# Performance work log

Measured on AMD Instinct MI355X. Metric: run time of the kernel, lower is better.

The kernel has to match this reference:

```python
import jax, jax.numpy as jnp
import numpy as np

REG_WEIGHT = 1e-4
N_LAYERS = 3


def setup_inputs() -> dict:
    key = jax.random.key(0)
    ks = jax.random.split(key, 7)
    n_users, n_items, d = 100000, 50000, 64
    E, B = 1600000, 4096
    return {
        "user_table": jax.random.normal(ks[0], (n_users, d), dtype=jnp.float32) * 0.01,
        "item_table": jax.random.normal(ks[1], (n_items, d), dtype=jnp.float32) * 0.01,
        "edge_u": jax.random.randint(ks[2], (E,), 0, n_users, dtype=jnp.int32),
        "edge_i": jax.random.randint(ks[3], (E,), 0, n_items, dtype=jnp.int32),
        "users": jax.random.randint(ks[4], (B,), 0, n_users, dtype=jnp.int32),
        "pos_items": jax.random.randint(ks[5], (B,), 0, n_items, dtype=jnp.int32),
        "neg_items": jax.random.randint(ks[6], (B,), 0, n_items, dtype=jnp.int32),
    }


def _lightgcn_embeddings(user_table, item_table, edge_u, edge_i):
    n_users, n_items = user_table.shape[0], item_table.shape[0]
    N = n_users + n_items
    E = edge_u.shape[0]
    ones = jnp.ones((E,), dtype=user_table.dtype)
    # symmetric normalization D^{-1/2} A D^{-1/2} on the bipartite graph
    deg_u = jax.ops.segment_sum(ones, edge_u, num_segments=n_users)
    deg_i = jax.ops.segment_sum(ones, edge_i, num_segments=n_items)
    w = jax.lax.rsqrt(jnp.maximum(deg_u[edge_u] * deg_i[edge_i], 1.0))
    # symmetric edge list over the stacked [users; items] node set
    rows = jnp.concatenate([edge_u, edge_i + n_users])
    cols = jnp.concatenate([edge_i + n_users, edge_u])
    vals = jnp.concatenate([w, w])[:, None]

    x = jnp.concatenate([user_table, item_table], axis=0)  # [N, d]
    acc = x
    for _ in range(N_LAYERS):
        x = jax.ops.segment_sum(x[cols] * vals, rows, num_segments=N)
        acc = acc + x
    final = acc / jnp.asarray(N_LAYERS + 1, dtype=x.dtype)
    return final[:n_users], final[n_users:]


def reference(user_table, item_table, edge_u, edge_i, users, pos_items, neg_items):
    user_emb_all, item_emb_all = _lightgcn_embeddings(user_table, item_table, edge_u, edge_i)
    u_emb = user_emb_all[users]
    pos_i_emb = item_emb_all[pos_items]
    neg_i_emb = item_emb_all[neg_items]
    pos_scores = jnp.sum(u_emb * pos_i_emb, axis=-1)
    neg_scores = jnp.sum(u_emb * neg_i_emb, axis=-1)
    # L2 regularization on the layer-0 (table) embeddings
    u0 = user_table[users]
    p0 = item_table[pos_items]
    n0 = item_table[neg_items]
    reg_loss = REG_WEIGHT * (jnp.sum(u0 * u0) + jnp.sum(p0 * p0) + jnp.sum(n0 * n0))
    reg_loss = reg_loss / users.shape[0]
    return pos_scores, neg_scores, reg_loss
```

## Files before the change

kernel.cpp:

```cpp
#include <hip/hip_runtime.h>
#include <hip/hip_fp16.h>

#define THREADS 256
#define BIN_C 4096
#define NBMAX 400
#define CAP 4608
#define SH_U 8
#define SH_I 7
#define CPAD 16
#define T_TILES 8
#define TSH_U 13
#define TSH_I 14

__global__ void bin_kernel(const int* __restrict__ eu, const int* __restrict__ ei,
                           int* __restrict__ bcnt_u, int* __restrict__ bcnt_i,
                           int* __restrict__ binu, int* __restrict__ bini,
                           int E, int nbu, int nbi) {
    __shared__ int hist_u[NBMAX], hist_i[NBMAX];
    __shared__ int base_u[NBMAX], base_i[NBMAX];
    int tid = threadIdx.x;
    int e0 = blockIdx.x * BIN_C;
    if (e0 >= E) return;
    int cnt = min(BIN_C, E - e0);

    for (int b = tid; b < NBMAX; b += THREADS) { hist_u[b] = 0; hist_i[b] = 0; }
    __syncthreads();

    int u[16], v[16];
    #pragma unroll
    for (int j = 0; j < 16; ++j) {
        int k = tid + j * THREADS;
        if (k < cnt) { u[j] = eu[e0 + k]; v[j] = ei[e0 + k]; }
        else         { u[j] = -1; v[j] = -1; }
    }
    #pragma unroll
    for (int j = 0; j < 16; ++j) {
        if (u[j] >= 0) {
            atomicAdd(&hist_u[u[j] >> SH_U], 1);
            atomicAdd(&hist_i[v[j] >> SH_I], 1);
        }
    }
    __syncthreads();
    for (int b = tid; b < NBMAX; b += THREADS) {
        int cu = hist_u[b], ci = hist_i[b];
        base_u[b] = (cu > 0 && b < nbu) ? atomicAdd(&bcnt_u[(size_t)b * CPAD], cu) : 0;
        base_i[b] = (ci > 0 && b < nbi) ? atomicAdd(&bcnt_i[(size_t)b * CPAD], ci) : 0;
        hist_u[b] = 0; hist_i[b] = 0;
    }
    __syncthreads();
    #pragma unroll
    for (int j = 0; j < 16; ++j) {
        if (u[j] >= 0) {
            int bu = u[j] >> SH_U;
            int pu = base_u[bu] + atomicAdd(&hist_u[bu], 1);
            if (pu < CAP) binu[(size_t)bu * CAP + pu] = ((u[j] & 255) << 16) | v[j];
            int bi = v[j] >> SH_I;
            int pi = base_i[bi] + atomicAdd(&hist_i[bi], 1);
            if (pi < CAP) bini[(size_t)bi * CAP + pi] = ((v[j] & 127) << 17) | u[j];
        }
    }
}

__global__ void place(const int* __restrict__ bcnt_u, const int* __restrict__ bcnt_i,
                      const int* __restrict__ binu, const int* __restrict__ bini,
                      int* __restrict__ offu, int* __restrict__ offi,
                      int* __restrict__ du, int* __restrict__ di,
                      float* __restrict__ rsdu, float* __restrict__ rsdi,
                      int* __restrict__ entu, int* __restrict__ enti,
                      int* __restrict__ curs,
                      int nbu, int nU, int nI) {
    __shared__ int stash[CAP];
    __shared__ int bin_cnt[THREADS * T_TILES];
    __shared__ int node_base[THREADS];
    __shared__ int wsum[4];
    __shared__ int bob_sh;
    int b = blockIdx.x;
    bool isU = (b < nbu);
    const int* bin; int base_node, nn, count;
    int *off, *deg, *ent; float* rsd;
    int losh, tsh, lomask;
    if (isU) {
        bin = binu + (size_t)b * CAP;
        base_node = b << SH_U; nn = min(256, nU - base_node);
        count = min(bcnt_u[(size_t)b * CPAD], CAP);
        off = offu; deg = du; rsd = rsdu; ent = entu;
        losh = 16; tsh = TSH_U; lomask = 0xFFFF;
    } else {
        int b2 = b - nbu;
        bin = bini + (size_t)b2 * CAP;
        base_node = b2 << SH_I; nn = min(128, nI - base_node);
        count = min(bcnt_i[(size_t)b2 * CPAD], CAP);
        off = offi; deg = di; rsd = rsdi; ent = enti;
        losh = 17; tsh = TSH_I; lomask = 0x1FFFF;
    }
    int tid = threadIdx.x;
    #pragma unroll
    for (int t = 0; t < T_TILES; ++t) bin_cnt[tid + t * THREADS] = 0;
    __syncthreads();
    for (int k = tid; k < count; k += THREADS) {
        int p = bin[k];
        stash[k] = p;
        int key = ((p >> losh) << 3) | ((p & lomask) >> tsh);
        atomicAdd(&bin_cnt[key], 1);
    }
    __syncthreads();
    int c = 0;
    {
        int base = tid * T_TILES;
        #pragma unroll
        for (int t = 0; t < T_TILES; ++t) {
            int v = bin_cnt[base + t];
            bin_cnt[base + t] = c;
            c += v;
        }
    }
    int seg = (c + 15) & ~15;
    int lane = tid & 63, wid = tid >> 6;
    int inc = seg;
    #pragma unroll
    for (int ofs = 1; ofs < 64; ofs <<= 1) {
        int t = __shfl_up(inc, ofs);
        if (lane >= ofs) inc += t;
    }
    if (lane == 63) wsum[wid] = inc;
    __syncthreads();
    int wofs = 0;
    #pragma unroll
    for (int w = 0; w < 4; ++w) wofs += (w < wid) ? wsum[w] : 0;
    int incl = inc + wofs;
    int excl = incl - seg;
    if (tid == THREADS - 1) bob_sh = atomicAdd(&curs[isU ? 0 : 1], incl);
    __syncthreads();
    int bob = bob_sh;
    node_base[tid] = excl;
    if (tid < nn) {
        off[base_node + tid] = bob + excl;
        deg[base_node + tid] = c;
        rsd[base_node + tid] = rsqrtf(fmaxf((float)c, 1.0f));
    }
    __syncthreads();
    #pragma unroll
    for (int t = 0; t < T_TILES; ++t) {
        int k = tid + t * THREADS;
        bin_cnt[k] += node_base[k >> 3];
    }
    __syncthreads();
    for (int k = tid; k < count; k += THREADS) {
        int p = stash[k];
        int key = ((p >> losh) << 3) | ((p & lomask) >> tsh);
        int sl = atomicAdd(&bin_cnt[key], 1);
        ent[bob + sl] = p & lomask;
    }
}

__global__ void conv16all(const float* __restrict__ ut, const float* __restrict__ it,
                          __half* __restrict__ dst, int nU16, int ntot16) {
    int stride = gridDim.x * blockDim.x;
    for (int i = blockIdx.x * blockDim.x + threadIdx.x; i < ntot16; i += stride) {
        const float* src = (i < nU16) ? (ut + (size_t)i * 4) : (it + (size_t)(i - nU16) * 4);
        float4 v = *reinterpret_cast<const float4*>(src);
        __half2 h0 = __float22half2_rn(make_float2(v.x, v.y));
        __half2 h1 = __float22half2_rn(make_float2(v.z, v.w));
        uint2 st;
        st.x = *reinterpret_cast<unsigned*>(&h0);
        st.y = *reinterpret_cast<unsigned*>(&h1);
        *reinterpret_cast<uint2*>(dst + (size_t)i * 4) = st;
    }
}

__global__ void prop16(const __half* __restrict__ x,
                       const int* __restrict__ offu, const int* __restrict__ offi,
                       const int* __restrict__ du, const int* __restrict__ di,
                       const float* __restrict__ rsdu, const float* __restrict__ rsdi,
                       const int* __restrict__ entu, const int* __restrict__ enti,
                       __half* __restrict__ y, int nU, int N) {
    int node = blockIdx.x * (THREADS >> 3) + (threadIdx.x >> 3);
    int lane = threadIdx.x & 7;
    if (node >= N) return;
    const int* ent; const __half* src; const float* rsdn;
    int beg, dg; float rs;
    if (node < nU) {
        beg = offu[node]; dg = du[node]; rs = rsdu[node];
        ent = entu; src = x + ((size_t)nU << 6); rsdn = rsdi;
    } else {
        int i = node - nU;
        beg = offi[i]; dg = di[i]; rs = rsdi[i];
        ent = enti; src = x; rsdn = rsdu;
    }
    float a0=0,a1=0,a2=0,a3=0,a4=0,a5=0,a6=0,a7=0;
    for (int k0 = 0; k0 < dg; k0 += 8) {
        int me = (k0 + lane < dg) ? ent[beg + k0 + lane] : 0;
        #pragma unroll
        for (int j = 0; j < 8; ++j) {
            if (k0 + j < dg) {
                int nbr = __shfl(me, j, 8);
                float w = rsdn[nbr];
                uint4 r = *reinterpret_cast<const uint4*>(src + ((size_t)nbr << 6) + (lane << 3));
                __half2 h0 = *reinterpret_cast<__half2*>(&r.x);
                __half2 h1 = *reinterpret_cast<__half2*>(&r.y);
                __half2 h2 = *reinterpret_cast<__half2*>(&r.z);
                __half2 h3 = *reinterpret_cast<__half2*>(&r.w);
                float2 f0 = __half22float2(h0), f1 = __half22float2(h1);
                float2 f2 = __half22float2(h2), f3 = __half22float2(h3);
                a0 += w * f0.x; a1 += w * f0.y; a2 += w * f1.x; a3 += w * f1.y;
                a4 += w * f2.x; a5 += w * f2.y; a6 += w * f3.x; a7 += w * f3.y;
            }
        }
    }
    __half2 o0 = __float22half2_rn(make_float2(a0 * rs, a1 * rs));
    __half2 o1 = __float22half2_rn(make_float2(a2 * rs, a3 * rs));
    __half2 o2 = __float22half2_rn(make_float2(a4 * rs, a5 * rs));
    __half2 o3 = __float22half2_rn(make_float2(a6 * rs, a7 * rs));
    uint4 st;
    st.x = *reinterpret_cast<unsigned*>(&o0);
    st.y = *reinterpret_cast<unsigned*>(&o1);
    st.z = *reinterpret_cast<unsigned*>(&o2);
    st.w = *reinterpret_cast<unsigned*>(&o3);
    *reinterpret_cast<uint4*>(y + ((size_t)node << 6) + (lane << 3)) = st;
}

__global__ void prop_sel_acc(const __half* __restrict__ x,
                             const int* __restrict__ users, const int* __restrict__ pos,
                             const int* __restrict__ neg,
                             const int* __restrict__ offu, const int* __restrict__ offi,
                             const int* __restrict__ du, const int* __restrict__ di,
                             const float* __restrict__ rsdu, const float* __restrict__ rsdi,
                             const int* __restrict__ entu, const int* __restrict__ enti,
                             float* __restrict__ sel, int B, int nU) {
    int r = blockIdx.x * (THREADS >> 3) + (threadIdx.x >> 3);
    int lane = threadIdx.x & 7;
    if (r >= 3 * B) return;
    int which = r / B, b = r - which * B;
    const int* ent; const __half* src; const float* rsdn;
    int beg, dg; float rs; size_t selfrow;
    if (which == 0) {
        int u = users[b];
        beg = offu[u]; dg = du[u]; rs = rsdu[u];
        ent = entu; src = x + ((size_t)nU << 6); rsdn = rsdi;
        selfrow = (size_t)u << 6;
    } else {
        int i = (which == 1) ? pos[b] : neg[b];
        beg = offi[i]; dg = di[i]; rs = rsdi[i];
        ent = enti; src = x; rsdn = rsdu;
        selfrow = (size_t)(nU + i) << 6;
    }
    float a0=0,a1=0,a2=0,a3=0,a4=0,a5=0,a6=0,a7=0;
    for (int k0 = 0; k0 < dg; k0 += 8) {
        int me = (k0 + lane < dg) ? ent[beg + k0 + lane] : 0;
        #pragma unroll
        for (int j = 0; j < 8; ++j) {
            if (k0 + j < dg) {
                int nbr = __shfl(me, j, 8);
                float w = rsdn[nbr];
                uint4 rv = *reinterpret_cast<const uint4*>(src + ((size_t)nbr << 6) + (lane << 3));
                __half2 h0 = *reinterpret_cast<__half2*>(&rv.x);
                __half2 h1 = *reinterpret_cast<__half2*>(&rv.y);
                __half2 h2 = *reinterpret_cast<__half2*>(&rv.z);
                __half2 h3 = *reinterpret_cast<__half2*>(&rv.w);
                float2 f0 = __half22float2(h0), f1 = __half22float2(h1);
                float2 f2 = __half22float2(h2), f3 = __half22float2(h3);
                a0 += w * f0.x; a1 += w * f0.y; a2 += w * f1.x; a3 += w * f1.y;
                a4 += w * f2.x; a5 += w * f2.y; a6 += w * f3.x; a7 += w * f3.y;
            }
        }
    }
    uint4 rv = *reinterpret_cast<const uint4*>(x + selfrow + (lane << 3));
    __half2 h0 = *reinterpret_cast<__half2*>(&rv.x);
    __half2 h1 = *reinterpret_cast<__half2*>(&rv.y);
    __half2 h2 = *reinterpret_cast<__half2*>(&rv.z);
    __half2 h3 = *reinterpret_cast<__half2*>(&rv.w);
    float2 s0 = __half22float2(h0), s1 = __half22float2(h1);
    float2 s2 = __half22float2(h2), s3 = __half22float2(h3);
    float* s = sel + ((size_t)r << 6) + (lane << 3);
    float4 d0 = *reinterpret_cast<float4*>(s);
    float4 d1 = *reinterpret_cast<float4*>(s + 4);
    d0.x += s0.x + rs * a0; d0.y += s0.y + rs * a1;
    d0.z += s1.x + rs * a2; d0.w += s1.y + rs * a3;
    d1.x += s2.x + rs * a4; d1.y += s2.y + rs * a5;
    d1.z += s3.x + rs * a6; d1.w += s3.y + rs * a7;
    *reinterpret_cast<float4*>(s) = d0;
    *reinterpret_cast<float4*>(s + 4) = d1;
}

__global__ void selreg(const float* __restrict__ ut, const float* __restrict__ it,
                       const int* __restrict__ users, const int* __restrict__ pos,
                       const int* __restrict__ neg,
                       float* __restrict__ sel, float* __restrict__ out_reg,
                       int B, float scale) {
    int r = blockIdx.x * (THREADS >> 4) + (threadIdx.x >> 4);
    int t = threadIdx.x & 15;
    float ssq = 0.f;
    if (r < 3 * B) {
        int which = r / B, b = r - which * B;
        const float* base; int idx;
        if (which == 0)      { base = ut; idx = users[b]; }
        else if (which == 1) { base = it; idx = pos[b]; }
        else                 { base = it; idx = neg[b]; }
        float4 v = *reinterpret_cast<const float4*>(base + ((size_t)idx << 6) + t * 4);
        *reinterpret_cast<float4*>(sel + ((size_t)r << 6) + t * 4) = v;
        ssq = v.x * v.x + v.y * v.y + v.z * v.z + v.w * v.w;
    }
    #pragma unroll
    for (int ofs = 32; ofs; ofs >>= 1) ssq += __shfl_down(ssq, ofs);
    if ((threadIdx.x & 63) == 0) atomicAdd(out_reg, ssq * scale);
}

__global__ void sel_acc16(const __half* __restrict__ x,
                          const int* __restrict__ users, const int* __restrict__ pos,
                          const int* __restrict__ neg, float* __restrict__ sel, int B, int nU) {
    int r = blockIdx.x * (THREADS >> 3) + (threadIdx.x >> 3);
    int lane = threadIdx.x & 7;
    if (r >= 3 * B) return;
    int which = r / B, b = r - which * B;
    size_t row;
    if (which == 0)      row = (size_t)users[b];
    else if (which == 1) row = (size_t)nU + pos[b];
    else                 row = (size_t)nU + neg[b];
    uint4 rv = *reinterpret_cast<const uint4*>(x + (row << 6) + (lane << 3));
    __half2 h0 = *reinterpret_cast<__half2*>(&rv.x);
    __half2 h1 = *reinterpret_cast<__half2*>(&rv.y);
    __half2 h2 = *reinterpret_cast<__half2*>(&rv.z);
    __half2 h3 = *reinterpret_cast<__half2*>(&rv.w);
    float2 f0 = __half22float2(h0), f1 = __half22float2(h1);
    float2 f2 = __half22float2(h2), f3 = __half22float2(h3);
    float* s = sel + ((size_t)r << 6) + (lane << 3);
    float4 d0 = *reinterpret_cast<float4*>(s);
    float4 d1 = *reinterpret_cast<float4*>(s + 4);
    d0.x += f0.x; d0.y += f0.y; d0.z += f1.x; d0.w += f1.y;
    d1.x += f2.x; d1.y += f2.y; d1.z += f3.x; d1.w += f3.y;
    *reinterpret_cast<float4*>(s) = d0;
    *reinterpret_cast<float4*>(s + 4) = d1;
}

__global__ void score(const float* __restrict__ sel, float* __restrict__ out, int B) {
    int b = blockIdx.x * (THREADS >> 6) + (threadIdx.x >> 6);
    int lane = threadIdx.x & 63;
    if (b >= B) return;
    float u = sel[((size_t)b << 6) + lane];
    float p = sel[((size_t)(B + b) << 6) + lane];
    float n = sel[((size_t)(2 * B + b) << 6) + lane];
    float ps = u * p, ns = u * n;
    for (int ofs = 32; ofs; ofs >>= 1) {
        ps += __shfl_down(ps, ofs);
        ns += __shfl_down(ns, ofs);
    }
    if (lane == 0) {
        out[b]     = ps * (1.0f / 16.0f);
        out[B + b] = ns * (1.0f / 16.0f);
    }
}

extern "C" void kernel_launch(void* const* d_in, const int* in_sizes, int n_in,
                              void* d_out, int out_size, void* d_ws, size_t ws_size,
                              hipStream_t stream) {
    const float* ut   = (const float*)d_in[0];
    const float* it   = (const float*)d_in[1];
    const int* eu     = (const int*)d_in[2];
    const int* ei     = (const int*)d_in[3];
    const int* users  = (const int*)d_in[4];
    const int* pos    = (const int*)d_in[5];
    const int* neg    = (const int*)d_in[6];
    int nU = in_sizes[0] / 64;
    int nI = in_sizes[1] / 64;
    int E  = in_sizes[2];
    int B  = in_sizes[4];
    int N  = nU + nI;
    float* out = (float*)d_out;

    int nbu = (nU + 255) >> SH_U;
    int nbi = (nI + 127) >> SH_I;

    char* ws = (char*)d_ws;
    size_t cursor = 0;
    auto alloc = [&](size_t bytes) -> void* {
        cursor = (cursor + 255) & ~(size_t)255;
        void* p = ws + cursor;
        cursor += bytes;
        return p;
    };
    int*   bcnt_u = (int*)alloc((size_t)nbu * CPAD * 4);
    int*   bcnt_i = (int*)alloc((size_t)nbi * CPAD * 4);
    int*   curs   = (int*)alloc(2 * 4);
    size_t zero_span = cursor;
    int*   binu = (int*)alloc((size_t)nbu * CAP * 4);
    int*   bini = (int*)alloc((size_t)nbi * CAP * 4);
    int*   offu = (int*)alloc((size_t)nU * 4);
    int*   offi = (int*)alloc((size_t)nI * 4);
    int*   du   = (int*)alloc((size_t)nU * 4);
    int*   di   = (int*)alloc((size_t)nI * 4);
    float* rsdu = (float*)alloc((size_t)nU * 4);
    float* rsdi = (float*)alloc((size_t)nI * 4);
    int*   entu = (int*)alloc(((size_t)E + (size_t)nbu * 256 * 16) * 4);
    int*   enti = (int*)alloc(((size_t)E + (size_t)nbi * 128 * 16) * 4);
    __half* xA  = (__half*)alloc((size_t)N * 64 * 2);
    __half* xB  = (__half*)alloc((size_t)N * 64 * 2);
    float* sel  = (float*)alloc((size_t)3 * B * 64 * 4);

    hipMemsetAsync(d_ws, 0, zero_span, stream);
    hipMemsetAsync(out + 2 * B, 0, sizeof(float), stream);

    conv16all<<<2048, THREADS, 0, stream>>>(ut, it, xA, nU * 16, N * 16);

    int nchunks = (E + BIN_C - 1) / BIN_C;
    bin_kernel<<<nchunks, THREADS, 0, stream>>>(eu, ei, bcnt_u, bcnt_i, binu, bini, E, nbu, nbi);
    place<<<nbu + nbi, THREADS, 0, stream>>>(bcnt_u, bcnt_i, binu, bini,
                                             offu, offi, du, di, rsdu, rsdi, entu, enti,
                                             curs, nbu, nU, nI);

    selreg<<<(3 * B + 15) / 16, THREADS, 0, stream>>>(ut, it, users, pos, neg, sel,
                                                      out + 2 * B, B, 1e-4f / (float)B);

    int gridSel16 = (3 * B * 8 + THREADS - 1) / THREADS;
    int gridProp = (N * 8 + THREADS - 1) / THREADS;
    prop16<<<gridProp, THREADS, 0, stream>>>(xA, offu, offi, du, di, rsdu, rsdi, entu, enti, xB, nU, N);
    sel_acc16<<<gridSel16, THREADS, 0, stream>>>(xB, users, pos, neg, sel, B, nU);
    prop16<<<gridProp, THREADS, 0, stream>>>(xB, offu, offi, du, di, rsdu, rsdi, entu, enti, xA, nU, N);
    prop_sel_acc<<<gridSel16, THREADS, 0, stream>>>(xA, users, pos, neg, offu, offi, du, di,
                                                    rsdu, rsdi, entu, enti, sel, B, nU);

    score<<<(B + 3) / 4, THREADS, 0, stream>>>(sel, out, B);
}
```

Measured before the change: 284.7 us.

## Fuse propagation layers and scoring into one cooperative kernel with grid syncs

Replaces the chain of prop16, sel_acc16, prop_sel_acc and score launches with a single persistent cooperative kernel that runs each phase in grid-stride loops and separates phases with grid.sync(). The second-layer select-accumulate now runs in the same phase as the second propagation. A separate bucket_off kernel computes per-bucket output offsets up front, and place uses a shared-memory scan instead of a per-block atomic cursor. This aims to remove kernel-launch gaps and tail effects between the short dependent stages, at the cost of grid-wide barrier overhead and a grid sized from occupancy queries, which may lower per-phase parallelism.

```diff
diff --git a/kernel.cpp b/kernel.cpp
--- a/kernel.cpp
+++ b/kernel.cpp
@@ -1,5 +1,8 @@
 #include <hip/hip_runtime.h>
 #include <hip/hip_fp16.h>
+#include <hip/hip_cooperative_groups.h>
+
+namespace cg = cooperative_groups;
 
 #define THREADS 256
 #define BIN_C 4096
@@ -11,147 +14,6 @@
 #define T_TILES 8
 #define TSH_U 13
 #define TSH_I 14
-
-__global__ void bin_kernel(const int* __restrict__ eu, const int* __restrict__ ei,
-                           int* __restrict__ bcnt_u, int* __restrict__ bcnt_i,
-                           int* __restrict__ binu, int* __restrict__ bini,
-                           int E, int nbu, int nbi) {
-    __shared__ int hist_u[NBMAX], hist_i[NBMAX];
-    __shared__ int base_u[NBMAX], base_i[NBMAX];
-    int tid = threadIdx.x;
-    int e0 = blockIdx.x * BIN_C;
-    if (e0 >= E) return;
-    int cnt = min(BIN_C, E - e0);
-
-    for (int b = tid; b < NBMAX; b += THREADS) { hist_u[b] = 0; hist_i[b] = 0; }
-    __syncthreads();
-
-    int u[16], v[16];
-    #pragma unroll
-    for (int j = 0; j < 16; ++j) {
-        int k = tid + j * THREADS;
-        if (k < cnt) { u[j] = eu[e0 + k]; v[j] = ei[e0 + k]; }
-        else         { u[j] = -1; v[j] = -1; }
-    }
-    #pragma unroll
-    for (int j = 0; j < 16; ++j) {
-        if (u[j] >= 0) {
-            atomicAdd(&hist_u[u[j] >> SH_U], 1);
-            atomicAdd(&hist_i[v[j] >> SH_I], 1);
-        }
-    }
-    __syncthreads();
-    for (int b = tid; b < NBMAX; b += THREADS) {
-        int cu = hist_u[b], ci = hist_i[b];
-        base_u[b] = (cu > 0 && b < nbu) ? atomicAdd(&bcnt_u[(size_t)b * CPAD], cu) : 0;
-        base_i[b] = (ci > 0 && b < nbi) ? atomicAdd(&bcnt_i[(size_t)b * CPAD], ci) : 0;
-        hist_u[b] = 0; hist_i[b] = 0;
-    }
-    __syncthreads();
-    #pragma unroll
-    for (int j = 0; j < 16; ++j) {
-        if (u[j] >= 0) {
-            int bu = u[j] >> SH_U;
-            int pu = base_u[bu] + atomicAdd(&hist_u[bu], 1);
-            if (pu < CAP) binu[(size_t)bu * CAP + pu] = ((u[j] & 255) << 16) | v[j];
-            int bi = v[j] >> SH_I;
-            int pi = base_i[bi] + atomicAdd(&hist_i[bi], 1);
-            if (pi < CAP) bini[(size_t)bi * CAP + pi] = ((v[j] & 127) << 17) | u[j];
-        }
-    }
-}
-
-__global__ void place(const int* __restrict__ bcnt_u, const int* __restrict__ bcnt_i,
-                      const int* __restrict__ binu, const int* __restrict__ bini,
-                      int* __restrict__ offu, int* __restrict__ offi,
-                      int* __restrict__ du, int* __restrict__ di,
-                      float* __restrict__ rsdu, float* __restrict__ rsdi,
-                      int* __restrict__ entu, int* __restrict__ enti,
-                      int* __restrict__ curs,
-                      int nbu, int nU, int nI) {
-    __shared__ int stash[CAP];
-    __shared__ int bin_cnt[THREADS * T_TILES];
-    __shared__ int node_base[THREADS];
-    __shared__ int wsum[4];
-    __shared__ int bob_sh;
-    int b = blockIdx.x;
-    bool isU = (b < nbu);
-    const int* bin; int base_node, nn, count;
-    int *off, *deg, *ent; float* rsd;
-    int losh, tsh, lomask;
-    if (isU) {
-        bin = binu + (size_t)b * CAP;
-        base_node = b << SH_U; nn = min(256, nU - base_node);
-        count = min(bcnt_u[(size_t)b * CPAD], CAP);
-        off = offu; deg = du; rsd = rsdu; ent = entu;
-        losh = 16; tsh = TSH_U; lomask = 0xFFFF;
-    } else {
-        int b2 = b - nbu;
-        bin = bini + (size_t)b2 * CAP;
-        base_node = b2 << SH_I; nn = min(128, nI - base_node);
-        count = min(bcnt_i[(size_t)b2 * CPAD], CAP);
-        off = offi; deg = di; rsd = rsdi; ent = enti;
-        losh = 17; tsh = TSH_I; lomask = 0x1FFFF;
-    }
-    int tid = threadIdx.x;
-    #pragma unroll
-    for (int t = 0; t < T_TILES; ++t) bin_cnt[tid + t * THREADS] = 0;
-    __syncthreads();
-    for (int k = tid; k < count; k += THREADS) {
-        int p = bin[k];
-        stash[k] = p;
-        int key = ((p >> losh) << 3) | ((p & lomask) >> tsh);
-        atomicAdd(&bin_cnt[key], 1);
-    }
-    __syncthreads();
-    int c = 0;
-    {
-        int base = tid * T_TILES;
-        #pragma unroll
-        for (int t = 0; t < T_TILES; ++t) {
-            int v = bin_cnt[base + t];
-            bin_cnt[base + t] = c;
-            c += v;
-        }
-    }
-    int seg = (c + 15) & ~15;
-    int lane = tid & 63, wid = tid >> 6;
-    int inc = seg;
-    #pragma unroll
-    for (int ofs = 1; ofs < 64; ofs <<= 1) {
-        int t = __shfl_up(inc, ofs);
-        if (lane >= ofs) inc += t;
-    }
-    if (lane == 63) wsum[wid] = inc;
-    __syncthreads();
-    int wofs = 0;
-    #pragma unroll
-    for (int w = 0; w < 4; ++w) wofs += (w < wid) ? wsum[w] : 0;
-    int incl = inc + wofs;
-    int excl = incl - seg;
-    if (tid == THREADS - 1) bob_sh = atomicAdd(&curs[isU ? 0 : 1], incl);
-    __syncthreads();
-    int bob = bob_sh;
-    node_base[tid] = excl;
-    if (tid < nn) {
-        off[base_node + tid] = bob + excl;
-        deg[base_node + tid] = c;
-        rsd[base_node + tid] = rsqrtf(fmaxf((float)c, 1.0f));
-    }
-    __syncthreads();
-    #pragma unroll
-    for (int t = 0; t < T_TILES; ++t) {
-        int k = tid + t * THREADS;
-        bin_cnt[k] += node_base[k >> 3];
-    }
-    __syncthreads();
-    for (int k = tid; k < count; k += THREADS) {
-        int p = stash[k];
-        int key = ((p >> losh) << 3) | ((p & lomask) >> tsh);
-        int sl = atomicAdd(&bin_cnt[key], 1);
-        ent[bob + sl] = p & lomask;
-    }
-}
 
 __global__ void conv16all(const float* __restrict__ ut, const float* __restrict__ it,
                           __half* __restrict__ dst, int nU16, int ntot16) {
@@ -168,15 +30,186 @@
     }
 }
 
-__global__ void prop16(const __half* __restrict__ x,
-                       const int* __restrict__ offu, const int* __restrict__ offi,
-                       const int* __restrict__ du, const int* __restrict__ di,
-                       const float* __restrict__ rsdu, const float* __restrict__ rsdi,
-                       const int* __restrict__ entu, const int* __restrict__ enti,
-                       __half* __restrict__ y, int nU, int N) {
-    int node = blockIdx.x * (THREADS >> 3) + (threadIdx.x >> 3);
-    int lane = threadIdx.x & 7;
-    if (node >= N) return;
+__global__ void bin_kernel(const int* __restrict__ eu, const int* __restrict__ ei,
+                           int* __restrict__ bcnt_u, int* __restrict__ bcnt_i,
+                           int* __restrict__ binu, int* __restrict__ bini,
+                           int E, int nbu, int nbi) {
+    __shared__ int hist_u[NBMAX], hist_i[NBMAX];
+    __shared__ int base_u[NBMAX], base_i[NBMAX];
+    int tid = threadIdx.x;
+    int e0 = blockIdx.x * BIN_C;
+    if (e0 >= E) return;
+    int cnt = min(BIN_C, E - e0);
+    for (int b = tid; b < NBMAX; b += THREADS) { hist_u[b] = 0; hist_i[b] = 0; }
+    __syncthreads();
+    int u[16], v[16];
+    #pragma unroll
+    for (int j = 0; j < 16; ++j) {
+        int k = tid + j * THREADS;
+        if (k < cnt) { u[j] = eu[e0 + k]; v[j] = ei[e0 + k]; }
+        else         { u[j] = -1; v[j] = -1; }
+    }
+    #pragma unroll
+    for (int j = 0; j < 16; ++j) {
+        if (u[j] >= 0) {
+            atomicAdd(&hist_u[u[j] >> SH_U], 1);
+            atomicAdd(&hist_i[v[j] >> SH_I], 1);
+        }
+    }
+    __syncthreads();
+    for (int b = tid; b < NBMAX; b += THREADS) {
+        int cu = hist_u[b], ci = hist_i[b];
+        base_u[b] = (cu > 0 && b < nbu) ? atomicAdd(&bcnt_u[(size_t)b * CPAD], cu) : 0;
+        base_i[b] = (ci > 0 && b < nbi) ? atomicAdd(&bcnt_i[(size_t)b * CPAD], ci) : 0;
+        hist_u[b] = 0; hist_i[b] = 0;
+    }
+    __syncthreads();
+    #pragma unroll
+    for (int j = 0; j < 16; ++j) {
+        if (u[j] >= 0) {
+            int bu = u[j] >> SH_U;
+            int pu = base_u[bu] + atomicAdd(&hist_u[bu], 1);
+            if (pu < CAP) binu[(size_t)bu * CAP + pu] = ((u[j] & 255) << 16) | v[j];
+            int bi = v[j] >> SH_I;
+            int pi = base_i[bi] + atomicAdd(&hist_i[bi], 1);
+            if (pi < CAP) bini[(size_t)bi * CAP + pi] = ((v[j] & 127) << 17) | u[j];
+        }
+    }
+}
+
+__global__ void bucket_off(const int* __restrict__ bcnt, int* __restrict__ bo,
+                           int* __restrict__ cursor, int nb, int pad) {
+    int idx = blockIdx.x * blockDim.x + threadIdx.x;
+    int lane = threadIdx.x & 63;
+    int d = 0;
+    if (idx < nb) d = min(bcnt[(size_t)idx * CPAD], CAP) + pad;
+    int s = d;
+    #pragma unroll
+    for (int ofs = 1; ofs < 64; ofs <<= 1) {
+        int t = __shfl_up(s, ofs);
+        if (lane >= ofs) s += t;
+    }
+    int total = __shfl(s, 63);
+    int base = 0;
+    if (lane == 63) base = atomicAdd(cursor, total);
+    base = __shfl(base, 63);
+    if (idx < nb) bo[idx] = base + s - d;
+}
+
+__global__ void place(const int* __restrict__ bcnt_u, const int* __restrict__ bcnt_i,
+                      const int* __restrict__ bo_u, const int* __restrict__ bo_i,
+                      const int* __restrict__ binu, const int* __restrict__ bini,
+                      int* __restrict__ offu, int* __restrict__ offi,
+                      int* __restrict__ du, int* __restrict__ di,
+                      float* __restrict__ rsdu, float* __restrict__ rsdi,
+                      int* __restrict__ entu, int* __restrict__ enti,
+                      int nbu, int nU, int nI) {
+    __shared__ int stash[CAP];
+    __shared__ int bin_cnt[THREADS * T_TILES];
+    __shared__ int scan[THREADS];
+    __shared__ int node_base[THREADS];
+    int b = blockIdx.x;
+    bool isU = (b < nbu);
+    const int* bin; int base_node, nn, count, bob;
+    int *off, *deg, *ent; float* rsd;
+    int losh, tsh;
+    if (isU) {
+        bin = binu + (size_t)b * CAP;
+        base_node = b << SH_U; nn = min(256, nU - base_node);
+        count = min(bcnt_u[(size_t)b * CPAD], CAP); bob = bo_u[b];
+        off = offu; deg = du; rsd = rsdu; ent = entu;
+        losh = 16; tsh = TSH_U;
+    } else {
+        int b2 = b - nbu;
+        bin = bini + (size_t)b2 * CAP;
+        base_node = b2 << SH_I; nn = min(128, nI - base_node);
+        count = min(bcnt_i[(size_t)b2 * CPAD], CAP); bob = bo_i[b2];
+        off = offi; deg = di; rsd = rsdi; ent = enti;
+        losh = 17; tsh = TSH_I;
+    }
+    int lomask = (1 << losh) - 1;
+    int tid = threadIdx.x;
+    #pragma unroll
+    for (int t = 0; t < T_TILES; ++t) bin_cnt[tid + t * THREADS] = 0;
+    __syncthreads();
+    for (int k = tid; k < count; k += THREADS) {
+        int p = bin[k];
+        stash[k] = p;
+        int key = ((p >> losh) << 3) | ((p & lomask) >> tsh);
+        atomicAdd(&bin_cnt[key], 1);
+    }
+    __syncthreads();
+    int c = 0;
+    {
+        int base = tid * T_TILES;
+        #pragma unroll
+        for (int t = 0; t < T_TILES; ++t) {
+            int v = bin_cnt[base + t];
+            bin_cnt[base + t] = c;
+            c += v;
+        }
+    }
+    int seg = (c + 15) & ~15;
+    scan[tid] = seg;
+    __syncthreads();
+    #pragma unroll
+    for (int ofs = 1; ofs < THREADS; ofs <<= 1) {
+        int t = (tid >= ofs) ? scan[tid - ofs] : 0;
+        __syncthreads();
+        scan[tid] += t;
+        __syncthreads();
+    }
+    int excl = scan[tid] - seg;
+    node_base[tid] = excl;
+    if (tid < nn) {
+        off[base_node + tid] = bob + excl;
+        deg[base_node + tid] = c;
+        rsd[base_node + tid] = rsqrtf(fmaxf((float)c, 1.0f));
+    }
+    __syncthreads();
+    #pragma unroll
+    for (int t = 0; t < T_TILES; ++t) {
+        int k = tid + t * THREADS;
+        bin_cnt[k] += node_base[k >> 3];
+    }
+    __syncthreads();
+    for (int k = tid; k < count; k += THREADS) {
+        int p = stash[k];
+        int key = ((p >> losh) << 3) | ((p & lomask) >> tsh);
+        int sl = atomicAdd(&bin_cnt[key], 1);
+        ent[bob + sl] = p & lomask;
+    }
+}
+
+__global__ void selreg(const float* __restrict__ ut, const float* __restrict__ it,
+                       const int* __restrict__ users, const int* __restrict__ pos,
+                       const int* __restrict__ neg,
+                       float* __restrict__ sel, float* __restrict__ out_reg,
+                       int B, float scale) {
+    int r = blockIdx.x * (THREADS >> 4) + (threadIdx.x >> 4);
+    int t = threadIdx.x & 15;
+    float ssq = 0.f;
+    if (r < 3 * B) {
+        int which = r / B, b = r - which * B;
+        const float* base; int idx;
+        if (which == 0)      { base = ut; idx = users[b]; }
+        else if (which == 1) { base = it; idx = pos[b]; }
+        else                 { base = it; idx = neg[b]; }
+        float4 v = *reinterpret_cast<const float4*>(base + ((size_t)idx << 6) + t * 4);
+        *reinterpret_cast<float4*>(sel + ((size_t)r << 6) + t * 4) = v;
+        ssq = v.x * v.x + v.y * v.y + v.z * v.z + v.w * v.w;
+    }
+    #pragma unroll
+    for (int ofs = 32; ofs; ofs >>= 1) ssq += __shfl_down(ssq, ofs);
+    if ((threadIdx.x & 63) == 0) atomicAdd(out_reg, ssq * scale);
+}
+
+__device__ __forceinline__ void prop_node(const __half* __restrict__ x,
+                                          const int* __restrict__ offu, const int* __restrict__ offi,
+                                          const int* __restrict__ du, const int* __restrict__ di,
+                                          const float* __restrict__ rsdu, const float* __restrict__ rsdi,
+                                          const int* __restrict__ entu, const int* __restrict__ enti,
+                                          __half* __restrict__ y, int nU, int node, int lane) {
     const int* ent; const __half* src; const float* rsdn;
     int beg, dg; float rs;
     if (node < nU) {
@@ -219,98 +252,10 @@
     *reinterpret_cast<uint4*>(y + ((size_t)node << 6) + (lane << 3)) = st;
 }
 
-__global__ void prop_sel_acc(const __half* __restrict__ x,
-                             const int* __restrict__ users, const int* __restrict__ pos,
-                             const int* __restrict__ neg,
-                             const int* __restrict__ offu, const int* __restrict__ offi,
-                             const int* __restrict__ du, const int* __restrict__ di,
-                             const float* __restrict__ rsdu, const float* __restrict__ rsdi,
-                             const int* __restrict__ entu, const int* __restrict__ enti,
-                             float* __restrict__ sel, int B, int nU) {
-    int r = blockIdx.x * (THREADS >> 3) + (threadIdx.x >> 3);
-    int lane = threadIdx.x & 7;
-    if (r >= 3 * B) return;
-    int which = r / B, b = r - which * B;
-    const int* ent; const __half* src; const float* rsdn;
-    int beg, dg; float rs; size_t selfrow;
-    if (which == 0) {
-        int u = users[b];
-        beg = offu[u]; dg = du[u]; rs = rsdu[u];
-        ent = entu; src = x + ((size_t)nU << 6); rsdn = rsdi;
-        selfrow = (size_t)u << 6;
-    } else {
-        int i = (which == 1) ? pos[b] : neg[b];
-        beg = offi[i]; dg = di[i]; rs = rsdi[i];
-        ent = enti; src = x; rsdn = rsdu;
-        selfrow = (size_t)(nU + i) << 6;
-    }
-    float a0=0,a1=0,a2=0,a3=0,a4=0,a5=0,a6=0,a7=0;
-    for (int k0 = 0; k0 < dg; k0 += 8) {
-        int me = (k0 + lane < dg) ? ent[beg + k0 + lane] : 0;
-        #pragma unroll
-        for (int j = 0; j < 8; ++j) {
-            if (k0 + j < dg) {
-                int nbr = __shfl(me, j, 8);
-                float w = rsdn[nbr];
-                uint4 rv = *reinterpret_cast<const uint4*>(src + ((size_t)nbr << 6) + (lane << 3));
-                __half2 h0 = *reinterpret_cast<__half2*>(&rv.x);
-                __half2 h1 = *reinterpret_cast<__half2*>(&rv.y);
-                __half2 h2 = *reinterpret_cast<__half2*>(&rv.z);
-                __half2 h3 = *reinterpret_cast<__half2*>(&rv.w);
-                float2 f0 = __half22float2(h0), f1 = __half22float2(h1);
-                float2 f2 = __half22float2(h2), f3 = __half22float2(h3);
-                a0 += w * f0.x; a1 += w * f0.y; a2 += w * f1.x; a3 += w * f1.y;
-                a4 += w * f2.x; a5 += w * f2.y; a6 += w * f3.x; a7 += w * f3.y;
-            }
-        }
-    }
-    uint4 rv = *reinterpret_cast<const uint4*>(x + selfrow + (lane << 3));
-    __half2 h0 = *reinterpret_cast<__half2*>(&rv.x);
-    __half2 h1 = *reinterpret_cast<__half2*>(&rv.y);
-    __half2 h2 = *reinterpret_cast<__half2*>(&rv.z);
-    __half2 h3 = *reinterpret_cast<__half2*>(&rv.w);
-    float2 s0 = __half22float2(h0), s1 = __half22float2(h1);
-    float2 s2 = __half22float2(h2), s3 = __half22float2(h3);
-    float* s = sel + ((size_t)r << 6) + (lane << 3);
-    float4 d0 = *reinterpret_cast<float4*>(s);
-    float4 d1 = *reinterpret_cast<float4*>(s + 4);
-    d0.x += s0.x + rs * a0; d0.y += s0.y + rs * a1;
-    d0.z += s1.x + rs * a2; d0.w += s1.y + rs * a3;
-    d1.x += s2.x + rs * a4; d1.y += s2.y + rs * a5;
-    d1.z += s3.x + rs * a6; d1.w += s3.y + rs * a7;
-    *reinterpret_cast<float4*>(s) = d0;
-    *reinterpret_cast<float4*>(s + 4) = d1;
-}
-
-__global__ void selreg(const float* __restrict__ ut, const float* __restrict__ it,
-                       const int* __restrict__ users, const int* __restrict__ pos,
-                       const int* __restrict__ neg,
-                       float* __restrict__ sel, float* __restrict__ out_reg,
-                       int B, float scale) {
-    int r = blockIdx.x * (THREADS >> 4) + (threadIdx.x >> 4);
-    int t = threadIdx.x & 15;
-    float ssq = 0.f;
-    if (r < 3 * B) {
-        int which = r / B, b = r - which * B;
-        const float* base; int idx;
-        if (which == 0)      { base = ut; idx = users[b]; }
-        else if (which == 1) { base = it; idx = pos[b]; }
-        else                 { base = it; idx = neg[b]; }
-        float4 v = *reinterpret_cast<const float4*>(base + ((size_t)idx << 6) + t * 4);
-        *reinterpret_cast<float4*>(sel + ((size_t)r << 6) + t * 4) = v;
-        ssq = v.x * v.x + v.y * v.y + v.z * v.z + v.w * v.w;
-    }
-    #pragma unroll
-    for (int ofs = 32; ofs; ofs >>= 1) ssq += __shfl_down(ssq, ofs);
-    if ((threadIdx.x & 63) == 0) atomicAdd(out_reg, ssq * scale);
-}
-
-__global__ void sel_acc16(const __half* __restrict__ x,
-                          const int* __restrict__ users, const int* __restrict__ pos,
-                          const int* __restrict__ neg, float* __restrict__ sel, int B, int nU) {
-    int r = blockIdx.x * (THREADS >> 3) + (threadIdx.x >> 3);
-    int lane = threadIdx.x & 7;
-    if (r >= 3 * B) return;
+__device__ __forceinline__ void selacc_row(const __half* __restrict__ x,
+                                           const int* __restrict__ users, const int* __restrict__ pos,
+                                           const int* __restrict__ neg,
+                                           float* __restrict__ sel, int B, int nU, int r, int lane) {
     int which = r / B, b = r - which * B;
     size_t row;
     if (which == 0)      row = (size_t)users[b];
@@ -332,21 +277,110 @@
     *reinterpret_cast<float4*>(s + 4) = d1;
 }
 
-__global__ void score(const float* __restrict__ sel, float* __restrict__ out, int B) {
-    int b = blockIdx.x * (THREADS >> 6) + (threadIdx.x >> 6);
-    int lane = threadIdx.x & 63;
-    if (b >= B) return;
-    float u = sel[((size_t)b << 6) + lane];
-    float p = sel[((size_t)(B + b) << 6) + lane];
-    float n = sel[((size_t)(2 * B + b) << 6) + lane];
-    float ps = u * p, ns = u * n;
-    for (int ofs = 32; ofs; ofs >>= 1) {
-        ps += __shfl_down(ps, ofs);
-        ns += __shfl_down(ns, ofs);
-    }
-    if (lane == 0) {
-        out[b]     = ps * (1.0f / 16.0f);
-        out[B + b] = ns * (1.0f / 16.0f);
+__device__ __forceinline__ void propselacc_row(const __half* __restrict__ x,
+                                               const int* __restrict__ users, const int* __restrict__ pos,
+                                               const int* __restrict__ neg,
+                                               const int* __restrict__ offu, const int* __restrict__ offi,
+                                               const int* __restrict__ du, const int* __restrict__ di,
+                                               const float* __restrict__ rsdu, const float* __restrict__ rsdi,
+                                               const int* __restrict__ entu, const int* __restrict__ enti,
+                                               float* __restrict__ sel, int B, int nU, int r, int lane) {
+    int which = r / B, b = r - which * B;
+    const int* ent; const __half* src; const float* rsdn;
+    int beg, dg; float rs; size_t selfrow;
+    if (which == 0) {
+        int u = users[b];
+        beg = offu[u]; dg = du[u]; rs = rsdu[u];
+        ent = entu; src = x + ((size_t)nU << 6); rsdn = rsdi;
+        selfrow = (size_t)u << 6;
+    } else {
+        int i = (which == 1) ? pos[b] : neg[b];
+        beg = offi[i]; dg = di[i]; rs = rsdi[i];
+        ent = enti; src = x; rsdn = rsdu;
+        selfrow = (size_t)(nU + i) << 6;
+    }
+    float a0=0,a1=0,a2=0,a3=0,a4=0,a5=0,a6=0,a7=0;
+    for (int k0 = 0; k0 < dg; k0 += 8) {
+        int me = (k0 + lane < dg) ? ent[beg + k0 + lane] : 0;
+        #pragma unroll
+        for (int j = 0; j < 8; ++j) {
+            if (k0 + j < dg) {
+                int nbr = __shfl(me, j, 8);
+                float w = rsdn[nbr];
+                uint4 rv = *reinterpret_cast<const uint4*>(src + ((size_t)nbr << 6) + (lane << 3));
+                __half2 h0 = *reinterpret_cast<__half2*>(&rv.x);
+                __half2 h1 = *reinterpret_cast<__half2*>(&rv.y);
+                __half2 h2 = *reinterpret_cast<__half2*>(&rv.z);
+                __half2 h3 = *reinterpret_cast<__half2*>(&rv.w);
+                float2 f0 = __half22float2(h0), f1 = __half22float2(h1);
+                float2 f2 = __half22float2(h2), f3 = __half22float2(h3);
+                a0 += w * f0.x; a1 += w * f0.y; a2 += w * f1.x; a3 += w * f1.y;
+                a4 += w * f2.x; a5 += w * f2.y; a6 += w * f3.x; a7 += w * f3.y;
+            }
+        }
+    }
+    uint4 rv = *reinterpret_cast<const uint4*>(x + selfrow + (lane << 3));
+    __half2 h0 = *reinterpret_cast<__half2*>(&rv.x);
+    __half2 h1 = *reinterpret_cast<__half2*>(&rv.y);
+    __half2 h2 = *reinterpret_cast<__half2*>(&rv.z);
+    __half2 h3 = *reinterpret_cast<__half2*>(&rv.w);
+    float2 s0 = __half22float2(h0), s1 = __half22float2(h1);
+    float2 s2 = __half22float2(h2), s3 = __half22float2(h3);
+    float* s = sel + ((size_t)r << 6) + (lane << 3);
+    float4 d0 = *reinterpret_cast<float4*>(s);
+    float4 d1 = *reinterpret_cast<float4*>(s + 4);
+    d0.x += s0.x + rs * a0; d0.y += s0.y + rs * a1;
+    d0.z += s1.x + rs * a2; d0.w += s1.y + rs * a3;
+    d1.x += s2.x + rs * a4; d1.y += s2.y + rs * a5;
+    d1.z += s3.x + rs * a6; d1.w += s3.y + rs * a7;
+    *reinterpret_cast<float4*>(s) = d0;
+    *reinterpret_cast<float4*>(s + 4) = d1;
+}
+
+__global__ __launch_bounds__(THREADS, 8)
+void coop_chain(__half* xA, __half* xB,
+                const int* offu, const int* offi, const int* du, const int* di,
+                const float* rsdu, const float* rsdi,
+                const int* entu, const int* enti,
+                const int* users, const int* pos, const int* neg,
+                float* sel, float* out, int B, int nU, int N) {
+    cg::grid_group grid = cg::this_grid();
+    int lane = threadIdx.x & 7;
+    int g0 = blockIdx.x * (THREADS >> 3) + (threadIdx.x >> 3);
+    int gs = gridDim.x * (THREADS >> 3);
+
+    for (int node = g0; node < N; node += gs)
+        prop_node(xA, offu, offi, du, di, rsdu, rsdi, entu, enti, xB, nU, node, lane);
+    grid.sync();
+
+    for (int node = g0; node < N; node += gs)
+        prop_node(xB, offu, offi, du, di, rsdu, rsdi, entu, enti, xA, nU, node, lane);
+    for (int r = g0; r < 3 * B; r += gs)
+        selacc_row(xB, users, pos, neg, sel, B, nU, r, lane);
+    grid.sync();
+
+    for (int r = g0; r < 3 * B; r += gs)
+        propselacc_row(xA, users, pos, neg, offu, offi, du, di, rsdu, rsdi,
+                       entu, enti, sel, B, nU, r, lane);
+    grid.sync();
+
+    int lane64 = threadIdx.x & 63;
+    int w0 = blockIdx.x * (THREADS >> 6) + (threadIdx.x >> 6);
+    int wsz = gridDim.x * (THREADS >> 6);
+    for (int b = w0; b < B; b += wsz) {
+        float u = sel[((size_t)b << 6) + lane64];
+        float p = sel[((size_t)(B + b) << 6) + lane64];
+        float n = sel[((size_t)(2 * B + b) << 6) + lane64];
+        float ps = u * p, ns = u * n;
+        #pragma unroll
+        for (int ofs = 32; ofs; ofs >>= 1) {
+            ps += __shfl_down(ps, ofs);
+            ns += __shfl_down(ns, ofs);
+        }
+        if (lane64 == 0) {
+            out[b]     = ps * (1.0f / 16.0f);
+            out[B + b] = ns * (1.0f / 16.0f);
+        }
     }
 }
 
@@ -369,6 +403,7 @@
 
     int nbu = (nU + 255) >> SH_U;
     int nbi = (nI + 127) >> SH_I;
+    int nchunks = (E + BIN_C - 1) / BIN_C;
 
     char* ws = (char*)d_ws;
     size_t cursor = 0;
@@ -382,6 +417,8 @@
     int*   bcnt_i = (int*)alloc((size_t)nbi * CPAD * 4);
     int*   curs   = (int*)alloc(2 * 4);
     size_t zero_span = cursor;
+    int*   bo_u = (int*)alloc((size_t)nbu * 4);
+    int*   bo_i = (int*)alloc((size_t)nbi * 4);
     int*   binu = (int*)alloc((size_t)nbu * CAP * 4);
     int*   bini = (int*)alloc((size_t)nbi * CAP * 4);
     int*   offu = (int*)alloc((size_t)nU * 4);
@@ -396,27 +433,34 @@
     __half* xB  = (__half*)alloc((size_t)N * 64 * 2);
     float* sel  = (float*)alloc((size_t)3 * B * 64 * 4);
 
-    hipMemsetAsync(d_ws, 0, zero_span, stream);
-    hipMemsetAsync(out + 2 * B, 0, sizeof(float), stream);
+    (void)hipMemsetAsync(d_ws, 0, zero_span, stream);
+    (void)hipMemsetAsync(out + 2 * B, 0, sizeof(float), stream);
 
     conv16all<<<2048, THREADS, 0, stream>>>(ut, it, xA, nU * 16, N * 16);
 
-    int nchunks = (E + BIN_C - 1) / BIN_C;
     bin_kernel<<<nchunks, THREADS, 0, stream>>>(eu, ei, bcnt_u, bcnt_i, binu, bini, E, nbu, nbi);
-    place<<<nbu + nbi, THREADS, 0, stream>>>(bcnt_u, bcnt_i, binu, bini,
+    bucket_off<<<(nbu + THREADS - 1) / THREADS, THREADS, 0, stream>>>(bcnt_u, bo_u, curs, nbu, 256 * 16);
+    bucket_off<<<(nbi + THREADS - 1) / THREADS, THREADS, 0, stream>>>(bcnt_i, bo_i, curs + 1, nbi, 128 * 16);
+    place<<<nbu + nbi, THREADS, 0, stream>>>(bcnt_u, bcnt_i, bo_u, bo_i, binu, bini,
                                              offu, offi, du, di, rsdu, rsdi, entu, enti,
-                                             curs, nbu, nU, nI);
+                                             nbu, nU, nI);
 
     selreg<<<(3 * B + 15) / 16, THREADS, 0, stream>>>(ut, it, users, pos, neg, sel,
                                                       out + 2 * B, B, 1e-4f / (float)B);
 
-    int gridSel16 = (3 * B * 8 + THREADS - 1) / THREADS;
-    int gridProp = (N * 8 + THREADS - 1) / THREADS;
-    prop16<<<gridProp, THREADS, 0, stream>>>(xA, offu, offi, du, di, rsdu, rsdi, entu, enti, xB, nU, N);
-    sel_acc16<<<gridSel16, THREADS, 0, stream>>>(xB, users, pos, neg, sel, B, nU);
-    prop16<<<gridProp, THREADS, 0, stream>>>(xB, offu, offi, du, di, rsdu, rsdi, entu, enti, xA, nU, N);
-    prop_sel_acc<<<gridSel16, THREADS, 0, stream>>>(xA, users, pos, neg, offu, offi, du, di,
-                                                    rsdu, rsdi, entu, enti, sel, B, nU);
-
-    score<<<(B + 3) / 4, THREADS, 0, stream>>>(sel, out, B);
-}
+    int perCU = 0;
+    if (hipOccupancyMaxActiveBlocksPerMultiprocessor(&perCU, (const void*)coop_chain, THREADS, 0)
+            != hipSuccess || perCU < 1)
+        perCU = 4;
+    int grid = perCU * 256;
+    if (grid > 2048) grid = 2048;
+    int needed = (N * 8 + THREADS - 1) / THREADS;
+    if (grid > needed) grid = needed;
+    float scaleB = 0.f; (void)scaleB;
+    void* args[] = { (void*)&xA, (void*)&xB, (void*)&offu, (void*)&offi, (void*)&du, (void*)&di,
+                     (void*)&rsdu, (void*)&rsdi, (void*)&entu, (void*)&enti,
+                     (void*)&users, (void*)&pos, (void*)&neg,
+                     (void*)&sel, (void*)&out, (void*)&B, (void*)&nU, (void*)&N };
+    (void)hipLaunchCooperativeKernel((const void*)coop_chain, dim3(grid), dim3(THREADS),
+                                     args, 0, stream);
+}
```

New measurement: 722.8 us. +153.9%, slower.
